# Kernel tuning notes

Measured on AMD Instinct MI355X. Metric: run time of the kernel, lower is better.

## Reference

```python
import jax, jax.numpy as jnp
import numpy as np

DIM = 2048
N_HEADS = 32
N_KV_HEADS = 8
HEAD_DIM = DIM // N_HEADS  # 64
GROUP = N_HEADS // N_KV_HEADS  # 4
ROPE_BASE = 10000.0


def setup_inputs() -> dict:
    key = jax.random.key(0)
    k1, k2, k3, k4, k5 = jax.random.split(key, 5)
    b, s = 1, 2048
    scale = 1.0 / np.sqrt(DIM)
    return {
        "x": jax.random.normal(k1, (b, s, DIM), dtype=jnp.float32),
        # weights stored as (in, out); equivalent math to torch Linear (x @ W.T)
        "wq": jax.random.normal(k2, (DIM, N_HEADS * HEAD_DIM), dtype=jnp.float32) * scale,
        "wk": jax.random.normal(k3, (DIM, N_KV_HEADS * HEAD_DIM), dtype=jnp.float32) * scale,
        "wv": jax.random.normal(k4, (DIM, N_KV_HEADS * HEAD_DIM), dtype=jnp.float32) * scale,
        "wo": jax.random.normal(k5, (N_HEADS * HEAD_DIM, DIM), dtype=jnp.float32) * scale,
    }


def _rope_cos_sin(seq_len, dtype):
    inv_freq = 1.0 / (ROPE_BASE ** (jnp.arange(0, HEAD_DIM, 2, dtype=jnp.float32) / HEAD_DIM))
    t = jnp.arange(seq_len, dtype=jnp.float32)
    freqs = jnp.outer(t, inv_freq)              # [s, hd/2]
    emb = jnp.concatenate([freqs, freqs], -1)   # [s, hd]
    return jnp.cos(emb).astype(dtype), jnp.sin(emb).astype(dtype)


def _rotate_half(x):
    x1, x2 = x[..., : HEAD_DIM // 2], x[..., HEAD_DIM // 2 :]
    return jnp.concatenate([-x2, x1], axis=-1)


def reference(x, wq, wk, wv, wo):
    b, s, _ = x.shape
    q = (x @ wq).reshape(b, s, N_HEADS, HEAD_DIM)
    k = (x @ wk).reshape(b, s, N_KV_HEADS, HEAD_DIM)
    v = (x @ wv).reshape(b, s, N_KV_HEADS, HEAD_DIM)

    cos, sin = _rope_cos_sin(s, x.dtype)
    cos = cos[None, :, None, :]  # [1, s, 1, hd] broadcast over batch & heads
    sin = sin[None, :, None, :]
    q = q * cos + _rotate_half(q) * sin
    k = k * cos + _rotate_half(k) * sin

    # GQA: repeat KV heads (repeat_interleave along head dim)
    k = jnp.repeat(k, GROUP, axis=2)  # [b, s, n_heads, hd]
    v = jnp.repeat(v, GROUP, axis=2)

    q = q.transpose(0, 2, 1, 3)  # [b, h, s, d]
    k = k.transpose(0, 2, 1, 3)
    v = v.transpose(0, 2, 1, 3)

    scores = jnp.einsum("bhqd,bhkd->bhqk", q, k) / jnp.sqrt(jnp.asarray(HEAD_DIM, x.dtype))
    attn = jax.nn.softmax(scores, axis=-1)
    out = jnp.einsum("bhqk,bhkd->bhqd", attn, v)
    out = out.transpose(0, 2, 1, 3).reshape(b, s, N_HEADS * HEAD_DIM)
    return out @ wo
```

## Files before the change

kernel.cpp:

```cpp
#include <hip/hip_runtime.h>
#include <hip/hip_bf16.h>

typedef __bf16 bf16x8 __attribute__((ext_vector_type(8)));
typedef __bf16 bf16x4 __attribute__((ext_vector_type(4)));
typedef float fx4 __attribute__((ext_vector_type(4)));
typedef float fx16 __attribute__((ext_vector_type(16)));

#define AS1 __attribute__((address_space(1)))
#define AS3 __attribute__((address_space(3)))

__global__ __launch_bounds__(256) void cast_x(const float4* __restrict__ X, __bf16* __restrict__ Xb) {
    int i = blockIdx.x * 256 + threadIdx.x;
    float4 v = X[i];
    bf16x4 o = { (__bf16)v.x, (__bf16)v.y, (__bf16)v.z, (__bf16)v.w };
    *(bf16x4*)(Xb + (size_t)i * 4) = o;
}

__global__ __launch_bounds__(256) void transpose_cast(const float* __restrict__ W, __bf16* __restrict__ Wt,
                                                      int K, int N) {
    __shared__ float t[32][33];
    const int tx = threadIdx.x & 31, ty = threadIdx.x >> 5;
    const int n0 = blockIdx.x * 32, k0 = blockIdx.y * 32;
#pragma unroll
    for (int i = 0; i < 4; ++i)
        t[ty + i * 8][tx] = W[(size_t)(k0 + ty + i * 8) * N + n0 + tx];
    __syncthreads();
#pragma unroll
    for (int i = 0; i < 4; ++i)
        Wt[(size_t)(n0 + ty + i * 8) * K + k0 + tx] = (__bf16)t[tx][ty + i * 8];
}

__global__ __launch_bounds__(256) void gemm_qkv(const __bf16* __restrict__ A, const __bf16* __restrict__ Bt,
                                                __bf16* __restrict__ Qr, __bf16* __restrict__ Kr,
                                                __bf16* __restrict__ Vt) {
    constexpr int K = 2048;
    __shared__ __align__(16) __bf16 lA[128 * 32];
    __shared__ __align__(16) __bf16 lB[128 * 32];
    const int tid = threadIdx.x;
    const int wave = tid >> 6, lane = tid & 63;
    const int quad = lane >> 4, l16 = lane & 15;
    const int m0 = blockIdx.x * 128, n0 = blockIdx.y * 128;
    const int wm = (wave >> 1) * 64, wn = (wave & 1) * 64;
    fx4 acc[4][4] = {};

    const int st0 = wave * 1024;
    const int st1 = 4096 + wave * 1024;
    const int r0 = (st0 + lane * 16) >> 6, c0 = ((st0 + lane * 16) & 63) >> 1;
    const int r1 = (st1 + lane * 16) >> 6, c1 = ((st1 + lane * 16) & 63) >> 1;

    for (int k0 = 0; k0 < K; k0 += 32) {
        __syncthreads();
        __builtin_amdgcn_global_load_lds((const AS1 void*)(A + (size_t)(m0 + r0) * K + k0 + c0),
                                         (AS3 void*)(lA + (st0 >> 1)), 16, 0, 0);
        __builtin_amdgcn_global_load_lds((const AS1 void*)(A + (size_t)(m0 + r1) * K + k0 + c1),
                                         (AS3 void*)(lA + (st1 >> 1)), 16, 0, 0);
        __builtin_amdgcn_global_load_lds((const AS1 void*)(Bt + (size_t)(n0 + r0) * K + k0 + c0),
                                         (AS3 void*)(lB + (st0 >> 1)), 16, 0, 0);
        __builtin_amdgcn_global_load_lds((const AS1 void*)(Bt + (size_t)(n0 + r1) * K + k0 + c1),
                                         (AS3 void*)(lB + (st1 >> 1)), 16, 0, 0);
        __builtin_amdgcn_s_waitcnt(0);
        __syncthreads();

        bf16x8 af[4], bfr[4];
#pragma unroll
        for (int i = 0; i < 4; ++i) af[i] = *(const bf16x8*)&lA[(wm + i * 16 + l16) * 32 + quad * 8];
#pragma unroll
        for (int j = 0; j < 4; ++j) bfr[j] = *(const bf16x8*)&lB[(wn + j * 16 + l16) * 32 + quad * 8];
#pragma unroll
        for (int i = 0; i < 4; ++i)
#pragma unroll
            for (int j = 0; j < 4; ++j)
                acc[i][j] = __builtin_amdgcn_mfma_f32_16x16x32_bf16(af[i], bfr[j], acc[i][j], 0, 0, 0);
    }

    const int col0 = n0 + wn;
    if (col0 < 2560) {
        const float scale = (col0 < 2048) ? 0.18033688011112042f : 1.0f;
        __bf16* base = (col0 < 2048) ? (Qr + (size_t)(col0 >> 6) * 2048 * 64)
                                     : (Kr + (size_t)((col0 - 2048) >> 6) * 2048 * 64);
#pragma unroll
        for (int jj = 0; jj < 2; ++jj) {
            const int dlo = jj * 16 + l16;
            const float inv = __builtin_amdgcn_exp2f(-(float)dlo * 0.41524101186092029f);
#pragma unroll
            for (int i = 0; i < 4; ++i)
#pragma unroll
                for (int r = 0; r < 4; ++r) {
                    const int s = m0 + wm + i * 16 + quad * 4 + r;
                    float sn, cs;
                    __sincosf((float)s * inv, &sn, &cs);
                    const float lo = acc[i][jj][r], hv = acc[i][jj + 2][r];
                    base[(size_t)s * 64 + dlo]      = (__bf16)((lo * cs - hv * sn) * scale);
                    base[(size_t)s * 64 + dlo + 32] = (__bf16)((hv * cs + lo * sn) * scale);
                }
        }
    } else {
        __bf16* vb = Vt + (size_t)((col0 - 2560) >> 6) * 64 * 2048;
#pragma unroll
        for (int i = 0; i < 4; ++i)
#pragma unroll
            for (int j = 0; j < 4; ++j) {
                const int d = j * 16 + l16;
                const int s0 = m0 + wm + i * 16 + quad * 4;
                bf16x4 p;
#pragma unroll
                for (int r = 0; r < 4; ++r) p[r] = (__bf16)acc[i][j][r];
                *(bf16x4*)&vb[(size_t)d * 2048 + s0] = p;
            }
    }
}

__global__ __launch_bounds__(256) void gemm_bt(const __bf16* __restrict__ A, const __bf16* __restrict__ Bt,
                                               float* __restrict__ C, int M, int N, int K) {
    __shared__ __align__(16) __bf16 lA[128 * 32];
    __shared__ __align__(16) __bf16 lB[128 * 32];
    const int tid = threadIdx.x;
    const int wave = tid >> 6, lane = tid & 63;
    const int quad = lane >> 4, l16 = lane & 15;
    const int m0 = blockIdx.x * 128, n0 = blockIdx.y * 128;
    const int wm = (wave >> 1) * 64, wn = (wave & 1) * 64;
    fx4 acc[4][4] = {};

    const int st0 = wave * 1024;
    const int st1 = 4096 + wave * 1024;
    const int r0 = (st0 + lane * 16) >> 6, c0 = ((st0 + lane * 16) & 63) >> 1;
    const int r1 = (st1 + lane * 16) >> 6, c1 = ((st1 + lane * 16) & 63) >> 1;

    for (int k0 = 0; k0 < K; k0 += 32) {
        __syncthreads();
        __builtin_amdgcn_global_load_lds((const AS1 void*)(A + (size_t)(m0 + r0) * K + k0 + c0),
                                         (AS3 void*)(lA + (st0 >> 1)), 16, 0, 0);
        __builtin_amdgcn_global_load_lds((const AS1 void*)(A + (size_t)(m0 + r1) * K + k0 + c1),
                                         (AS3 void*)(lA + (st1 >> 1)), 16, 0, 0);
        __builtin_amdgcn_global_load_lds((const AS1 void*)(Bt + (size_t)(n0 + r0) * K + k0 + c0),
                                         (AS3 void*)(lB + (st0 >> 1)), 16, 0, 0);
        __builtin_amdgcn_global_load_lds((const AS1 void*)(Bt + (size_t)(n0 + r1) * K + k0 + c1),
                                         (AS3 void*)(lB + (st1 >> 1)), 16, 0, 0);
        __builtin_amdgcn_s_waitcnt(0);
        __syncthreads();

        bf16x8 af[4], bfr[4];
#pragma unroll
        for (int i = 0; i < 4; ++i) af[i] = *(const bf16x8*)&lA[(wm + i * 16 + l16) * 32 + quad * 8];
#pragma unroll
        for (int j = 0; j < 4; ++j) bfr[j] = *(const bf16x8*)&lB[(wn + j * 16 + l16) * 32 + quad * 8];
#pragma unroll
        for (int i = 0; i < 4; ++i)
#pragma unroll
            for (int j = 0; j < 4; ++j)
                acc[i][j] = __builtin_amdgcn_mfma_f32_16x16x32_bf16(af[i], bfr[j], acc[i][j], 0, 0, 0);
    }
#pragma unroll
    for (int i = 0; i < 4; ++i)
#pragma unroll
        for (int j = 0; j < 4; ++j) {
            const int row = m0 + wm + i * 16 + quad * 4;
            const int col = n0 + wn + j * 16 + l16;
#pragma unroll
            for (int r = 0; r < 4; ++r)
                C[(size_t)(row + r) * N + col] = acc[i][j][r];
        }
}

__global__ __launch_bounds__(256, 2) void flash_attn(const __bf16* __restrict__ Qr, const __bf16* __restrict__ Kr,
                                                     const __bf16* __restrict__ Vt, __bf16* __restrict__ O) {
    constexpr int S = 2048;
    __shared__ __align__(16) __bf16 lK[64 * 72];
    __shared__ __align__(16) __bf16 lV[64 * 72];
    __shared__ __align__(16) __bf16 lP[4][32 * 72];
    const int qt = blockIdx.x, h = blockIdx.y, kvh = h >> 2;
    const int tid = threadIdx.x, wave = tid >> 6, lane = tid & 63;
    const int l32 = lane & 31, hi = lane >> 5;

    const int qrow = qt * 128 + wave * 32 + l32;
    const __bf16* qptr = Qr + ((size_t)h * S + qrow) * 64;
    bf16x8 qf[4];
#pragma unroll
    for (int kc = 0; kc < 4; ++kc) qf[kc] = *(const bf16x8*)(qptr + kc * 16 + hi * 8);

    const __bf16* Kbase = Kr + (size_t)kvh * S * 64;
    const __bf16* Vbase = Vt + (size_t)kvh * 64 * S;

    const int krow = tid >> 3;
    const int kcol = (tid & 7) * 8;

    bf16x8 kreg0 = *(const bf16x8*)(Kbase + (size_t)krow * 64 + kcol);
    bf16x8 kreg1 = *(const bf16x8*)(Kbase + (size_t)(32 + krow) * 64 + kcol);
    bf16x8 vreg0 = *(const bf16x8*)(Vbase + (size_t)krow * S + kcol);
    bf16x8 vreg1 = *(const bf16x8*)(Vbase + (size_t)(32 + krow) * S + kcol);

    fx16 ov0, ov1;
#pragma unroll
    for (int i = 0; i < 16; ++i) { ov0[i] = 0.f; ov1[i] = 0.f; }
    float l_acc = 0.f;
    __bf16* lPw = &lP[wave][0];

    for (int kt = 0; kt < S / 64; ++kt) {
        __syncthreads();
        *(bf16x8*)&lK[krow * 72 + kcol] = kreg0;
        *(bf16x8*)&lK[(32 + krow) * 72 + kcol] = kreg1;
        *(bf16x8*)&lV[krow * 72 + kcol] = vreg0;
        *(bf16x8*)&lV[(32 + krow) * 72 + kcol] = vreg1;
        const int ktn = (kt + 1 < S / 64) ? kt + 1 : kt;
        kreg0 = *(const bf16x8*)(Kbase + (size_t)(ktn * 64 + krow) * 64 + kcol);
        kreg1 = *(const bf16x8*)(Kbase + (size_t)(ktn * 64 + 32 + krow) * 64 + kcol);
        vreg0 = *(const bf16x8*)(Vbase + (size_t)krow * S + ktn * 64 + kcol);
        vreg1 = *(const bf16x8*)(Vbase + (size_t)(32 + krow) * S + ktn * 64 + kcol);
        __syncthreads();

        fx16 sc0, sc1;
#pragma unroll
        for (int i = 0; i < 16; ++i) { sc0[i] = 0.f; sc1[i] = 0.f; }
#pragma unroll
        for (int kc = 0; kc < 4; ++kc) {
            const bf16x8 a0 = *(const bf16x8*)&lK[l32 * 72 + kc * 16 + hi * 8];
            const bf16x8 a1 = *(const bf16x8*)&lK[(32 + l32) * 72 + kc * 16 + hi * 8];
            sc0 = __builtin_amdgcn_mfma_f32_32x32x16_bf16(a0, qf[kc], sc0, 0, 0, 0);
            sc1 = __builtin_amdgcn_mfma_f32_32x32x16_bf16(a1, qf[kc], sc1, 0, 0, 0);
        }

#pragma unroll
        for (int mt = 0; mt < 2; ++mt) {
#pragma unroll
            for (int rg2 = 0; rg2 < 4; ++rg2) {
                bf16x4 pk;
#pragma unroll
                for (int r = 0; r < 4; ++r) {
                    const float p = __builtin_amdgcn_exp2f(mt ? sc1[rg2 * 4 + r] : sc0[rg2 * 4 + r]);
                    l_acc += p;
                    pk[r] = (__bf16)p;
                }
                *(bf16x4*)&lPw[l32 * 72 + mt * 32 + rg2 * 8 + hi * 4] = pk;
            }
        }

#pragma unroll
        for (int kc = 0; kc < 4; ++kc) {
            const bf16x8 pb = *(const bf16x8*)&lPw[l32 * 72 + kc * 16 + hi * 8];
            const bf16x8 va0 = *(const bf16x8*)&lV[l32 * 72 + kc * 16 + hi * 8];
            const bf16x8 va1 = *(const bf16x8*)&lV[(32 + l32) * 72 + kc * 16 + hi * 8];
            ov0 = __builtin_amdgcn_mfma_f32_32x32x16_bf16(va0, pb, ov0, 0, 0, 0);
            ov1 = __builtin_amdgcn_mfma_f32_32x32x16_bf16(va1, pb, ov1, 0, 0, 0);
        }
    }

    const float l_tot = l_acc + __shfl_xor(l_acc, 32, 64);
    const float inv_l = 1.0f / l_tot;

#pragma unroll
    for (int dt = 0; dt < 2; ++dt)
#pragma unroll
        for (int rg2 = 0; rg2 < 4; ++rg2) {
            bf16x4 o4;
#pragma unroll
            for (int r = 0; r < 4; ++r)
                o4[r] = (__bf16)((dt ? ov1[rg2 * 4 + r] : ov0[rg2 * 4 + r]) * inv_l);
            const int col = h * 64 + dt * 32 + rg2 * 8 + hi * 4;
            *(bf16x4*)(O + (size_t)qrow * 2048 + col) = o4;
        }
}

extern "C" void kernel_launch(void* const* d_in, const int* in_sizes, int n_in,
                              void* d_out, int out_size, void* d_ws, size_t ws_size,
                              hipStream_t stream) {
    const float* x  = (const float*)d_in[0];
    const float* wq = (const float*)d_in[1];
    const float* wk = (const float*)d_in[2];
    const float* wv = (const float*)d_in[3];
    const float* wo = (const float*)d_in[4];
    float* out = (float*)d_out;
    char* ws = (char*)d_ws;

    __bf16* Xb    = (__bf16*)ws;
    __bf16* WqkvT = (__bf16*)(ws + ((size_t)8 << 20));
    __bf16* WoT   = (__bf16*)(ws + ((size_t)20 << 20));
    __bf16* Qr    = (__bf16*)(ws + ((size_t)28 << 20));
    __bf16* Kr    = (__bf16*)(ws + ((size_t)36 << 20));
    __bf16* Vt    = (__bf16*)(ws + ((size_t)38 << 20));
    __bf16* Ob    = (__bf16*)(ws + ((size_t)40 << 20));

    cast_x<<<4096, 256, 0, stream>>>((const float4*)x, Xb);
    transpose_cast<<<dim3(64, 64), 256, 0, stream>>>(wq, WqkvT, 2048, 2048);
    transpose_cast<<<dim3(16, 64), 256, 0, stream>>>(wk, WqkvT + (size_t)2048 * 2048, 2048, 512);
    transpose_cast<<<dim3(16, 64), 256, 0, stream>>>(wv, WqkvT + (size_t)2560 * 2048, 2048, 512);
    transpose_cast<<<dim3(64, 64), 256, 0, stream>>>(wo, WoT, 2048, 2048);

    gemm_qkv<<<dim3(16, 24), 256, 0, stream>>>(Xb, WqkvT, Qr, Kr, Vt);
    flash_attn<<<dim3(16, 32), 256, 0, stream>>>(Qr, Kr, Vt, Ob);
    gemm_bt<<<dim3(16, 16), 256, 0, stream>>>(Ob, WoT, out, 2048, 2048, 2048);
}
```

Baseline: 244.2 us.

## Merge weight transposes, shrink QKV tiles, split-K output projection

Folds the four weight transpose launches into one kernel that picks its matrix by block index. The QKV GEMM now uses 128x64 tiles, giving 768 blocks instead of 384 so more CUs have work. The output projection is split over K into two halves written to separate buffers and then summed by a reduce kernel, which doubles the number of blocks. The cost is extra float traffic for the partial buffer and one more launch. The partial buffer reuses the workspace area that held Xb, which is dead by that point.

Result: faster. 231.0 us (-5.4%).

```diff
diff --git a/kernel.cpp b/kernel.cpp
--- a/kernel.cpp
+++ b/kernel.cpp
@@ -16,11 +16,19 @@
     *(bf16x4*)(Xb + (size_t)i * 4) = o;
 }
 
-__global__ __launch_bounds__(256) void transpose_cast(const float* __restrict__ W, __bf16* __restrict__ Wt,
-                                                      int K, int N) {
+__global__ __launch_bounds__(256) void transpose_all(const float* __restrict__ wq, const float* __restrict__ wk,
+                                                     const float* __restrict__ wv, const float* __restrict__ wo,
+                                                     __bf16* __restrict__ WqkvT, __bf16* __restrict__ WoT) {
+    constexpr int K = 2048;
     __shared__ float t[32][33];
+    const int bx = blockIdx.x;
+    const float* W; __bf16* Wt; int N, n0;
+    if (bx < 64)      { W = wq; Wt = WqkvT;                        N = 2048; n0 = bx * 32; }
+    else if (bx < 80) { W = wk; Wt = WqkvT + (size_t)2048 * 2048;  N = 512;  n0 = (bx - 64) * 32; }
+    else if (bx < 96) { W = wv; Wt = WqkvT + (size_t)2560 * 2048;  N = 512;  n0 = (bx - 80) * 32; }
+    else              { W = wo; Wt = WoT;                          N = 2048; n0 = (bx - 96) * 32; }
     const int tx = threadIdx.x & 31, ty = threadIdx.x >> 5;
-    const int n0 = blockIdx.x * 32, k0 = blockIdx.y * 32;
+    const int k0 = blockIdx.y * 32;
 #pragma unroll
     for (int i = 0; i < 4; ++i)
         t[ty + i * 8][tx] = W[(size_t)(k0 + ty + i * 8) * N + n0 + tx];
@@ -34,12 +42,103 @@
                                                 __bf16* __restrict__ Qr, __bf16* __restrict__ Kr,
                                                 __bf16* __restrict__ Vt) {
     constexpr int K = 2048;
+    __shared__ __align__(16) __bf16 lA[128 * 32];
+    __shared__ __align__(16) __bf16 lB[64 * 32];
+    const int tid = threadIdx.x;
+    const int wave = tid >> 6, lane = tid & 63;
+    const int quad = lane >> 4, l16 = lane & 15;
+    const int m0 = blockIdx.x * 128, n0 = blockIdx.y * 64;
+    fx4 acc[2][4] = {};
+
+    int cr[3], cc[3];
+    const __bf16* csrc[3];
+    __bf16* cdst[3];
+#pragma unroll
+    for (int it = 0; it < 3; ++it) {
+        const int c = wave * 3 + it;
+        if (c < 8) {
+            const int boff = c * 1024 + lane * 16;
+            cr[it] = boff >> 6; cc[it] = (boff & 63) >> 1;
+            csrc[it] = A + (size_t)(m0 + cr[it]) * K;
+            cdst[it] = lA + c * 512;
+        } else {
+            const int boff = (c - 8) * 1024 + lane * 16;
+            cr[it] = boff >> 6; cc[it] = (boff & 63) >> 1;
+            csrc[it] = Bt + (size_t)(n0 + cr[it]) * K;
+            cdst[it] = lB + (c - 8) * 512;
+        }
+    }
+
+    for (int k0 = 0; k0 < K; k0 += 32) {
+        __syncthreads();
+#pragma unroll
+        for (int it = 0; it < 3; ++it)
+            __builtin_amdgcn_global_load_lds((const AS1 void*)(csrc[it] + k0 + cc[it]),
+                                             (AS3 void*)cdst[it], 16, 0, 0);
+        __builtin_amdgcn_s_waitcnt(0);
+        __syncthreads();
+
+        bf16x8 af[2], bfr[4];
+#pragma unroll
+        for (int i = 0; i < 2; ++i) af[i] = *(const bf16x8*)&lA[(wave * 32 + i * 16 + l16) * 32 + quad * 8];
+#pragma unroll
+        for (int j = 0; j < 4; ++j) bfr[j] = *(const bf16x8*)&lB[(j * 16 + l16) * 32 + quad * 8];
+#pragma unroll
+        for (int i = 0; i < 2; ++i)
+#pragma unroll
+            for (int j = 0; j < 4; ++j)
+                acc[i][j] = __builtin_amdgcn_mfma_f32_16x16x32_bf16(af[i], bfr[j], acc[i][j], 0, 0, 0);
+    }
+
+    const int by = blockIdx.y;
+    if (by < 40) {
+        const float scale = (by < 32) ? 0.18033688011112042f : 1.0f;
+        __bf16* base = (by < 32) ? (Qr + (size_t)by * 2048 * 64)
+                                 : (Kr + (size_t)(by - 32) * 2048 * 64);
+#pragma unroll
+        for (int jj = 0; jj < 2; ++jj) {
+            const int dlo = jj * 16 + l16;
+            const float inv = __builtin_amdgcn_exp2f(-(float)dlo * 0.41524101186092029f);
+#pragma unroll
+            for (int i = 0; i < 2; ++i)
+#pragma unroll
+                for (int r = 0; r < 4; ++r) {
+                    const int s = m0 + wave * 32 + i * 16 + quad * 4 + r;
+                    float sn, cs;
+                    __sincosf((float)s * inv, &sn, &cs);
+                    const float lo = acc[i][jj][r], hv = acc[i][jj + 2][r];
+                    base[(size_t)s * 64 + dlo]      = (__bf16)((lo * cs - hv * sn) * scale);
+                    base[(size_t)s * 64 + dlo + 32] = (__bf16)((hv * cs + lo * sn) * scale);
+                }
+        }
+    } else {
+        __bf16* vb = Vt + (size_t)(by - 40) * 64 * 2048;
+#pragma unroll
+        for (int i = 0; i < 2; ++i)
+#pragma unroll
+            for (int j = 0; j < 4; ++j) {
+                const int d = j * 16 + l16;
+                const int s0 = m0 + wave * 32 + i * 16 + quad * 4;
+                bf16x4 p;
+#pragma unroll
+                for (int r = 0; r < 4; ++r) p[r] = (__bf16)acc[i][j][r];
+                *(bf16x4*)&vb[(size_t)d * 2048 + s0] = p;
+            }
+    }
+}
+
+__global__ __launch_bounds__(256) void gemm_bt_sk(const __bf16* __restrict__ A, const __bf16* __restrict__ Bt,
+                                                  float* __restrict__ C0, float* __restrict__ C1,
+                                                  int M, int N, int K) {
     __shared__ __align__(16) __bf16 lA[128 * 32];
     __shared__ __align__(16) __bf16 lB[128 * 32];
     const int tid = threadIdx.x;
     const int wave = tid >> 6, lane = tid & 63;
     const int quad = lane >> 4, l16 = lane & 15;
     const int m0 = blockIdx.x * 128, n0 = blockIdx.y * 128;
+    const int kz = blockIdx.z;
+    const int kbeg = kz * (K >> 1), kend = kbeg + (K >> 1);
+    float* C = kz ? C1 : C0;
     const int wm = (wave >> 1) * 64, wn = (wave & 1) * 64;
     fx4 acc[4][4] = {};
 
@@ -48,7 +147,7 @@
     const int r0 = (st0 + lane * 16) >> 6, c0 = ((st0 + lane * 16) & 63) >> 1;
     const int r1 = (st1 + lane * 16) >> 6, c1 = ((st1 + lane * 16) & 63) >> 1;
 
-    for (int k0 = 0; k0 < K; k0 += 32) {
+    for (int k0 = kbeg; k0 < kend; k0 += 32) {
         __syncthreads();
         __builtin_amdgcn_global_load_lds((const AS1 void*)(A + (size_t)(m0 + r0) * K + k0 + c0),
                                          (AS3 void*)(lA + (st0 >> 1)), 16, 0, 0);
@@ -72,84 +171,6 @@
             for (int j = 0; j < 4; ++j)
                 acc[i][j] = __builtin_amdgcn_mfma_f32_16x16x32_bf16(af[i], bfr[j], acc[i][j], 0, 0, 0);
     }
-
-    const int col0 = n0 + wn;
-    if (col0 < 2560) {
-        const float scale = (col0 < 2048) ? 0.18033688011112042f : 1.0f;
-        __bf16* base = (col0 < 2048) ? (Qr + (size_t)(col0 >> 6) * 2048 * 64)
-                                     : (Kr + (size_t)((col0 - 2048) >> 6) * 2048 * 64);
-#pragma unroll
-        for (int jj = 0; jj < 2; ++jj) {
-            const int dlo = jj * 16 + l16;
-            const float inv = __builtin_amdgcn_exp2f(-(float)dlo * 0.41524101186092029f);
-#pragma unroll
-            for (int i = 0; i < 4; ++i)
-#pragma unroll
-                for (int r = 0; r < 4; ++r) {
-                    const int s = m0 + wm + i * 16 + quad * 4 + r;
-                    float sn, cs;
-                    __sincosf((float)s * inv, &sn, &cs);
-                    const float lo = acc[i][jj][r], hv = acc[i][jj + 2][r];
-                    base[(size_t)s * 64 + dlo]      = (__bf16)((lo * cs - hv * sn) * scale);
-                    base[(size_t)s * 64 + dlo + 32] = (__bf16)((hv * cs + lo * sn) * scale);
-                }
-        }
-    } else {
-        __bf16* vb = Vt + (size_t)((col0 - 2560) >> 6) * 64 * 2048;
-#pragma unroll
-        for (int i = 0; i < 4; ++i)
-#pragma unroll
-            for (int j = 0; j < 4; ++j) {
-                const int d = j * 16 + l16;
-                const int s0 = m0 + wm + i * 16 + quad * 4;
-                bf16x4 p;
-#pragma unroll
-                for (int r = 0; r < 4; ++r) p[r] = (__bf16)acc[i][j][r];
-                *(bf16x4*)&vb[(size_t)d * 2048 + s0] = p;
-            }
-    }
-}
-
-__global__ __launch_bounds__(256) void gemm_bt(const __bf16* __restrict__ A, const __bf16* __restrict__ Bt,
-                                               float* __restrict__ C, int M, int N, int K) {
-    __shared__ __align__(16) __bf16 lA[128 * 32];
-    __shared__ __align__(16) __bf16 lB[128 * 32];
-    const int tid = threadIdx.x;
-    const int wave = tid >> 6, lane = tid & 63;
-    const int quad = lane >> 4, l16 = lane & 15;
-    const int m0 = blockIdx.x * 128, n0 = blockIdx.y * 128;
-    const int wm = (wave >> 1) * 64, wn = (wave & 1) * 64;
-    fx4 acc[4][4] = {};
-
-    const int st0 = wave * 1024;
-    const int st1 = 4096 + wave * 1024;
-    const int r0 = (st0 + lane * 16) >> 6, c0 = ((st0 + lane * 16) & 63) >> 1;
-    const int r1 = (st1 + lane * 16) >> 6, c1 = ((st1 + lane * 16) & 63) >> 1;
-
-    for (int k0 = 0; k0 < K; k0 += 32) {
-        __syncthreads();
-        __builtin_amdgcn_global_load_lds((const AS1 void*)(A + (size_t)(m0 + r0) * K + k0 + c0),
-                                         (AS3 void*)(lA + (st0 >> 1)), 16, 0, 0);
-        __builtin_amdgcn_global_load_lds((const AS1 void*)(A + (size_t)(m0 + r1) * K + k0 + c1),
-                                         (AS3 void*)(lA + (st1 >> 1)), 16, 0, 0);
-        __builtin_amdgcn_global_load_lds((const AS1 void*)(Bt + (size_t)(n0 + r0) * K + k0 + c0),
-                                         (AS3 void*)(lB + (st0 >> 1)), 16, 0, 0);
-        __builtin_amdgcn_global_load_lds((const AS1 void*)(Bt + (size_t)(n0 + r1) * K + k0 + c1),
-                                         (AS3 void*)(lB + (st1 >> 1)), 16, 0, 0);
-        __builtin_amdgcn_s_waitcnt(0);
-        __syncthreads();
-
-        bf16x8 af[4], bfr[4];
-#pragma unroll
-        for (int i = 0; i < 4; ++i) af[i] = *(const bf16x8*)&lA[(wm + i * 16 + l16) * 32 + quad * 8];
-#pragma unroll
-        for (int j = 0; j < 4; ++j) bfr[j] = *(const bf16x8*)&lB[(wn + j * 16 + l16) * 32 + quad * 8];
-#pragma unroll
-        for (int i = 0; i < 4; ++i)
-#pragma unroll
-            for (int j = 0; j < 4; ++j)
-                acc[i][j] = __builtin_amdgcn_mfma_f32_16x16x32_bf16(af[i], bfr[j], acc[i][j], 0, 0, 0);
-    }
 #pragma unroll
     for (int i = 0; i < 4; ++i)
 #pragma unroll
@@ -160,6 +181,14 @@
             for (int r = 0; r < 4; ++r)
                 C[(size_t)(row + r) * N + col] = acc[i][j][r];
         }
+}
+
+__global__ __launch_bounds__(256) void reduce_add(float4* __restrict__ out, const float4* __restrict__ p) {
+    const int i = blockIdx.x * 256 + threadIdx.x;
+    float4 a = out[i];
+    const float4 b = p[i];
+    a.x += b.x; a.y += b.y; a.z += b.z; a.w += b.w;
+    out[i] = a;
 }
 
 __global__ __launch_bounds__(256, 2) void flash_attn(const __bf16* __restrict__ Qr, const __bf16* __restrict__ Kr,
@@ -278,14 +307,13 @@
     __bf16* Kr    = (__bf16*)(ws + ((size_t)36 << 20));
     __bf16* Vt    = (__bf16*)(ws + ((size_t)38 << 20));
     __bf16* Ob    = (__bf16*)(ws + ((size_t)40 << 20));
+    float*  Cp    = (float*)ws;
 
     cast_x<<<4096, 256, 0, stream>>>((const float4*)x, Xb);
-    transpose_cast<<<dim3(64, 64), 256, 0, stream>>>(wq, WqkvT, 2048, 2048);
-    transpose_cast<<<dim3(16, 64), 256, 0, stream>>>(wk, WqkvT + (size_t)2048 * 2048, 2048, 512);
-    transpose_cast<<<dim3(16, 64), 256, 0, stream>>>(wv, WqkvT + (size_t)2560 * 2048, 2048, 512);
-    transpose_cast<<<dim3(64, 64), 256, 0, stream>>>(wo, WoT, 2048, 2048);
-
-    gemm_qkv<<<dim3(16, 24), 256, 0, stream>>>(Xb, WqkvT, Qr, Kr, Vt);
+    transpose_all<<<dim3(160, 64), 256, 0, stream>>>(wq, wk, wv, wo, WqkvT, WoT);
+
+    gemm_qkv<<<dim3(16, 48), 256, 0, stream>>>(Xb, WqkvT, Qr, Kr, Vt);
     flash_attn<<<dim3(16, 32), 256, 0, stream>>>(Qr, Kr, Vt, Ob);
-    gemm_bt<<<dim3(16, 16), 256, 0, stream>>>(Ob, WoT, out, 2048, 2048, 2048);
-}
+    gemm_bt_sk<<<dim3(16, 16, 2), 256, 0, stream>>>(Ob, WoT, out, Cp, 2048, 2048, 2048);
+    reduce_add<<<4096, 256, 0, stream>>>((float4*)out, (const float4*)Cp);
+}
```
